# Performance work log

Hardware: AMD Instinct MI355X
Metric: run time of the kernel (lower is better)

The kernel has to match this reference:

```python
import jax, jax.numpy as jnp
import numpy as np

H, DK, OUT = 8, 32, 256
SQRT_DK = float(np.sqrt(DK))


def _proj(feat, W, b):
    # (N, in) -> (N, H, DK)
    return (feat @ W + b).reshape(feat.shape[0], H, DK)


def _rel(k_src, v_src, q_dst, src, dst, att_w, msg_w, pri, n_dst):
    # HGT-style per-relation edge attention + segment softmax + aggregation.
    key = jnp.einsum('ehd,hdk->ehk', k_src[src], att_w)          # (E,H,DK)
    att = (q_dst[dst] * key).sum(-1) * pri / SQRT_DK             # (E,H)
    val = jnp.einsum('ehd,hdk->ehk', v_src[src], msg_w)          # (E,H,DK)
    m = jax.ops.segment_max(att, dst, num_segments=n_dst)
    m = jnp.where(jnp.isfinite(m), m, 0.0)
    e = jnp.exp(att - m[dst])
    s = jax.ops.segment_sum(e, dst, num_segments=n_dst)
    alpha = e / jnp.maximum(s[dst], 1e-9)
    h = jax.ops.segment_sum(alpha[..., None] * val, dst, num_segments=n_dst)
    return jax.nn.relu(h.reshape(n_dst, OUT))                    # relu per etype (reduce_func)


def _ln(x, g, b):
    mu = x.mean(-1, keepdims=True)
    var = ((x - mu) ** 2).mean(-1, keepdims=True)
    return (x - mu) / jnp.sqrt(var + 1e-5) * g + b


def _forward(feat_word, feat_topic, feat_doc, Wk, bk, Wq, bq, Wv, bv, Wa, ba,
             ln_scale, ln_bias, skip, rel_pri, rel_att, rel_msg,
             src_ww, dst_ww, src_wt, dst_wt, src_wd, dst_wd,
             src_tt, dst_tt, src_td, dst_td):
    # ntype order: word=0, topic=1, doc=2; etype order: ww=0, wt=1, wd=2, tt=3, td=4
    Nw, Nt, Nd = feat_word.shape[0], feat_topic.shape[0], feat_doc.shape[0]
    k_w, q_w, v_w = _proj(feat_word, Wk[0], bk[0]), _proj(feat_word, Wq[0], bq[0]), _proj(feat_word, Wv[0], bv[0])
    k_t, q_t, v_t = _proj(feat_topic, Wk[1], bk[1]), _proj(feat_topic, Wq[1], bq[1]), _proj(feat_topic, Wv[1], bv[1])
    q_d = _proj(feat_doc, Wq[2], bq[2])
    t_ww = _rel(k_w, v_w, q_w, src_ww, dst_ww, rel_att[0], rel_msg[0], rel_pri[0], Nw)
    t_wt = _rel(k_w, v_w, q_t, src_wt, dst_wt, rel_att[1], rel_msg[1], rel_pri[1], Nt)
    t_wd = _rel(k_w, v_w, q_d, src_wd, dst_wd, rel_att[2], rel_msg[2], rel_pri[2], Nd)
    t_tt = _rel(k_t, v_t, q_t, src_tt, dst_tt, rel_att[3], rel_msg[3], rel_pri[3], Nt)
    t_td = _rel(k_t, v_t, q_d, src_td, dst_td, rel_att[4], rel_msg[4], rel_pri[4], Nd)
    # cross_reducer='mean' across etypes targeting each ntype
    t_word, t_topic, t_doc = t_ww, (t_wt + t_tt) * 0.5, (t_wd + t_td) * 0.5
    outs = []
    for i, (t, feat) in enumerate([(t_word, feat_word), (t_topic, feat_topic), (t_doc, feat_doc)]):
        a = jax.nn.sigmoid(skip[i])
        trans = (t @ Wa[i] + ba[i]) * a + feat * (1.0 - a)
        outs.append(_ln(trans, ln_scale[i], ln_bias[i]))
    return jnp.concatenate(outs, axis=0)  # (Nw+Nt+Nd, OUT)


def setup_inputs() -> dict:
    key = jax.random.key(0)
    ks = jax.random.split(key, 32)
    Nw, Nt, Nd, D = 20000, 2000, 5000, 256
    E = {'ww': (150000, Nw, Nw), 'wt': (80000, Nw, Nt), 'wd': (80000, Nw, Nd),
         'tt': (20000, Nt, Nt), 'td': (40000, Nt, Nd)}
    inp = {
        'feat_word': jax.random.normal(ks[0], (Nw, D), jnp.float32),
        'feat_topic': jax.random.normal(ks[1], (Nt, D), jnp.float32),
        'feat_doc': jax.random.normal(ks[2], (Nd, D), jnp.float32),
        'Wk': jax.random.normal(ks[3], (3, D, D), jnp.float32) * 0.05,
        'bk': jax.random.normal(ks[4], (3, D), jnp.float32) * 0.02,
        'Wq': jax.random.normal(ks[5], (3, D, D), jnp.float32) * 0.05,
        'bq': jax.random.normal(ks[6], (3, D), jnp.float32) * 0.02,
        'Wv': jax.random.normal(ks[7], (3, D, D), jnp.float32) * 0.05,
        'bv': jax.random.normal(ks[8], (3, D), jnp.float32) * 0.02,
        'Wa': jax.random.normal(ks[9], (3, D, D), jnp.float32) * 0.05,
        'ba': jax.random.normal(ks[10], (3, D), jnp.float32) * 0.02,
        'ln_scale': jnp.ones((3, D), jnp.float32),
        'ln_bias': jnp.zeros((3, D), jnp.float32),
        'skip': jnp.ones((3,), jnp.float32),
        'rel_pri': jnp.ones((5, H), jnp.float32),
        'rel_att': jax.random.normal(ks[11], (5, H, DK, DK), jnp.float32) * 0.1,
        'rel_msg': jax.random.normal(ks[12], (5, H, DK, DK), jnp.float32) * 0.1,
    }
    for i, (et, (ne, ns, nd)) in enumerate(E.items()):
        inp['src_' + et] = jax.random.randint(ks[13 + 2 * i], (ne,), 0, ns, jnp.int32)
        inp['dst_' + et] = jax.random.randint(ks[14 + 2 * i], (ne,), 0, nd, jnp.int32)
    return inp


def reference(feat_word, feat_topic, feat_doc, Wk, bk, Wq, bq, Wv, bv, Wa, ba,
              ln_scale, ln_bias, skip, rel_pri, rel_att, rel_msg,
              src_ww, dst_ww, src_wt, dst_wt, src_wd, dst_wd,
              src_tt, dst_tt, src_td, dst_td):
    return _forward(feat_word, feat_topic, feat_doc, Wk, bk, Wq, bq, Wv, bv, Wa, ba,
                    ln_scale, ln_bias, skip, rel_pri, rel_att, rel_msg,
                    src_ww, dst_ww, src_wt, dst_wt, src_wd, dst_wd,
                    src_tt, dst_tt, src_td, dst_td)
```

## Files before the change

### kernel.cpp

```cpp
#include <hip/hip_runtime.h>

static constexpr int NW = 20000, NT = 2000, ND = 5000;
static constexpr int E_WW = 150000, E_WT = 80000, E_WD = 80000, E_TT = 20000, E_TD = 40000;

typedef short bf16x8 __attribute__((ext_vector_type(8)));
typedef float f32x4 __attribute__((ext_vector_type(4)));
typedef float f32x2 __attribute__((ext_vector_type(2)));

__device__ __forceinline__ unsigned short f2bf(float f) {
  union { float f; unsigned int u; } c; c.f = f;
  unsigned int u = c.u;
  u += 0x7fffu + ((u >> 16) & 1u);
  return (unsigned short)(u >> 16);
}
__device__ __forceinline__ float bf2f(unsigned short h) {
  union { unsigned int u; float f; } c; c.u = ((unsigned int)h) << 16; return c.f;
}
__device__ __forceinline__ bf16x8 pack8(float4 a, float4 b) {
  bf16x8 r;
  r[0] = (short)f2bf(a.x); r[1] = (short)f2bf(a.y); r[2] = (short)f2bf(a.z); r[3] = (short)f2bf(a.w);
  r[4] = (short)f2bf(b.x); r[5] = (short)f2bf(b.y); r[6] = (short)f2bf(b.z); r[7] = (short)f2bf(b.w);
  return r;
}
__device__ __forceinline__ unsigned char f2fp8(float x) {
  int p = __builtin_amdgcn_cvt_pk_fp8_f32(x, x, 0, false);
  return (unsigned char)(p & 0xff);
}

struct CsrDesc {
  const int* dst[5];
  const int* src[5];
  int E[5], N[5], cbase[5];
};

struct PrepArgs {
  const float* psrc[7]; unsigned short* pdst[7];
  const float* wq[5]; const float* bqp[5];
  unsigned short* qdst[5];
  float* beff;
  const float* att;
  const float* msg; unsigned short* wvp;
  CsrDesc dsc;
  int* counts;
  int bEff, bHw, bHist, bTot;
};
__global__ __launch_bounds__(256) void prep_kernel(PrepArgs a) {
  __shared__ float tile[32][33];
  int b = blockIdx.x;
  int tid = threadIdx.x;
  if (b < a.bEff) {
    int m = b >> 6, bk = ((b >> 3) & 7) * 32, bn = (b & 7) * 32;
    const float* W = a.psrc[m];
    unsigned short* WT = a.pdst[m];
    int tx = tid & 31, ty = tid >> 5;
#pragma unroll
    for (int i = 0; i < 32; i += 8)
      tile[ty + i][tx] = W[(size_t)(bk + ty + i) * 256 + bn + tx];
    __syncthreads();
#pragma unroll
    for (int i = 0; i < 32; i += 8)
      WT[(size_t)(bn + ty + i) * 256 + bk + tx] = f2bf(tile[tx][ty + i]);
  } else if (b < a.bHw) {
    int t = (b - a.bEff) * 256 + tid;
    if (t < 5 * 65536) {
      int r = t >> 16, rem = t & 65535;
      int n = rem >> 8, kk = rem & 255;
      int h = n >> 5, j = n & 31;
      const float* wrow = a.wq[r] + kk * 256 + h * 32;
      const float* arow = a.att + r * 8192 + h * 1024 + j * 32;
      float s = 0.f;
#pragma unroll
      for (int d = 0; d < 32; d += 4) {
        float4 wv = *(const float4*)(wrow + d);
        float4 av = *(const float4*)(arow + d);
        s += wv.x * av.x + wv.y * av.y + wv.z * av.z + wv.w * av.w;
      }
      a.qdst[r][n * 256 + kk] = f2bf(s);
    } else {
      int idx = t - 5 * 65536;
      if (idx < 1280) {
        int r = idx >> 8, n = idx & 255;
        int h = n >> 5, j = n & 31;
        const float* brow = a.bqp[r] + h * 32;
        const float* arow = a.att + r * 8192 + h * 1024 + j * 32;
        float s = 0.f;
#pragma unroll
        for (int d = 0; d < 32; d += 4) {
          float4 bv = *(const float4*)(brow + d);
          float4 av = *(const float4*)(arow + d);
          s += bv.x * av.x + bv.y * av.y + bv.z * av.z + bv.w * av.w;
        }
        a.beff[r * 256 + n] = s;
      }
    }
  } else if (b < a.bHist) {
    int t = (b - a.bHw) * 256 + tid;
    if (t < 5 * 8192) {
      int m = t >> 13, rem = t & 8191;
      int hc = rem >> 9, idx = rem & 511;
      int lane = idx >> 3, j = idx & 7;
      int h = hc >> 1, c = hc & 1;
      int k = (lane >> 4) * 8 + j, n = c * 16 + (lane & 15);
      a.wvp[t] = f2bf(a.msg[(size_t)m * 8192 + h * 1024 + k * 32 + n]);
    }
  } else {
    int t = (b - a.bHist) * 256 + tid;
    int r = 0, base = 0;
    while (r < 5 && t >= base + a.dsc.E[r]) { base += a.dsc.E[r]; r++; }
    if (r >= 5) return;
    int e = t - base;
    atomicAdd(a.counts + a.dsc.cbase[r] + a.dsc.dst[r][e], 1);
  }
}

struct ProjAll {
  const float* A[3];
  const unsigned short* WT[3];
  const float* bias[3][4];
  unsigned char* outB[3][4];
  int esz[3][4];
  int M[3], ncolb[3], bcum[4];
  const int* counts; int* offsets; int scanN;
};
__global__ __launch_bounds__(256) void proj_all(ProjAll pa) {
  __shared__ unsigned short As[64 * 64];
  __shared__ unsigned short Bs[64 * 64];
  __shared__ int wpart2[4];
  __shared__ int carry2;
  const int tid = threadIdx.x;
  if ((int)blockIdx.x >= pa.bcum[3]) {
    int lane = tid & 63, w = tid >> 6;
    if (tid == 0) carry2 = 0;
    __syncthreads();
    const int N = pa.scanN;
    for (int base = 0; base < N; base += 1024) {
      int idx = base + tid * 4;
      int v0 = 0, v1 = 0, v2 = 0, v3 = 0;
      if (idx + 3 < N) {
        int4 t4 = *(const int4*)(pa.counts + idx);
        v0 = t4.x; v1 = t4.y; v2 = t4.z; v3 = t4.w;
      } else if (idx < N) {
        v0 = pa.counts[idx];
        if (idx + 1 < N) v1 = pa.counts[idx + 1];
        if (idx + 2 < N) v2 = pa.counts[idx + 2];
      }
      int ts = v0 + v1 + v2 + v3;
      int x = ts;
#pragma unroll
      for (int d = 1; d < 64; d <<= 1) {
        int t = __shfl_up(x, d, 64);
        if (lane >= d) x += t;
      }
      if (lane == 63) wpart2[w] = x;
      __syncthreads();
      if (tid == 0) {
        int s = 0;
#pragma unroll
        for (int j = 0; j < 4; j++) { int t = wpart2[j]; wpart2[j] = s; s += t; }
      }
      __syncthreads();
      int excl = carry2 + wpart2[w] + (x - ts);
      if (idx < N)     pa.offsets[idx]     = excl;
      if (idx + 1 < N) pa.offsets[idx + 1] = excl + v0;
      if (idx + 2 < N) pa.offsets[idx + 2] = excl + v0 + v1;
      if (idx + 3 < N) pa.offsets[idx + 3] = excl + v0 + v1 + v2;
      __syncthreads();
      if (tid == 255) carry2 = excl + ts;
      __syncthreads();
    }
    if (tid == 0) pa.offsets[N] = carry2;
    return;
  }
  int nt = 0;
  while (nt < 2 && (int)blockIdx.x >= pa.bcum[nt + 1]) nt++;
  int local = blockIdx.x - pa.bcum[nt];
  int ncolb = pa.ncolb[nt];
  int bmi = local / ncolb, bnb = local % ncolb;
  const int bm = bmi * 64, bn = bnb * 64;
  const float* A = pa.A[nt];
  const unsigned short* WT = pa.WT[nt];
  const int M = pa.M[nt];
  const int wave = tid >> 6, lane = tid & 63;
  f32x4 acc[4] = {};
  const int ar = wave * 16 + (lane & 15);
  const int swz = lane & 7;
  for (int k0 = 0; k0 < 256; k0 += 64) {
#pragma unroll
    for (int i = 0; i < 2; i++) {
      int c = tid + i * 256;
      int row = c >> 3, sl = c & 7;
      int srow = bm + row;
      float4 a0 = make_float4(0.f, 0.f, 0.f, 0.f), a1 = a0;
      if (srow < M) {
        a0 = *(const float4*)(A + (size_t)srow * 256 + k0 + sl * 8);
        a1 = *(const float4*)(A + (size_t)srow * 256 + k0 + sl * 8 + 4);
      }
      *(bf16x8*)&As[row * 64 + (sl ^ (row & 7)) * 8] = pack8(a0, a1);
      bf16x8 bv = *(const bf16x8*)(WT + (size_t)(bn + row) * 256 + k0 + sl * 8);
      *(bf16x8*)&Bs[row * 64 + (sl ^ (row & 7)) * 8] = bv;
    }
    __syncthreads();
#pragma unroll
    for (int kk = 0; kk < 2; kk++) {
      int slot = kk * 4 + (lane >> 4);
      bf16x8 av = *(const bf16x8*)&As[ar * 64 + ((slot ^ swz) * 8)];
#pragma unroll
      for (int nf = 0; nf < 4; nf++) {
        int br = nf * 16 + (lane & 15);
        bf16x8 bv = *(const bf16x8*)&Bs[br * 64 + ((slot ^ swz) * 8)];
        acc[nf] = __builtin_amdgcn_mfma_f32_16x16x32_bf16(av, bv, acc[nf], 0, 0, 0);
      }
    }
    __syncthreads();
  }
  const int col = lane & 15;
  const int seg = bnb >> 2;
  const float* bias = pa.bias[nt][seg];
  unsigned char* outB = pa.outB[nt][seg];
  const int esz = pa.esz[nt][seg];
  const int cbase = (bnb & 3) * 64;
#pragma unroll
  for (int nf = 0; nf < 4; nf++) {
    float bsv = bias[cbase + nf * 16 + col];
    int idx = cbase + nf * 16 + col;
#pragma unroll
    for (int rr = 0; rr < 4; rr++) {
      int row = bm + wave * 16 + (lane >> 4) * 4 + rr;
      if (row < M) {
        float v = acc[nf][rr] + bsv;
        if (esz == 2) *(unsigned short*)(outB + (size_t)row * 512 + idx * 2) = f2bf(v);
        else          outB[(size_t)row * 512 + idx] = f2fp8(v);
      }
    }
  }
}

__global__ void scatter5(CsrDesc d, const int* __restrict__ offsets, int* __restrict__ cursor,
                         int* __restrict__ ssrc) {
  int t = blockIdx.x * blockDim.x + threadIdx.x;
  int r = 0, base = 0;
  while (r < 5 && t >= base + d.E[r]) { base += d.E[r]; r++; }
  if (r >= 5) return;
  int e = t - base;
  int dn = d.dst[r][e];
  int pos = offsets[d.cbase[r] + dn] + atomicAdd(cursor + d.cbase[r] + dn, 1);
  ssrc[pos] = d.src[r][e];
}

struct AttArgs {
  const unsigned short* qh[5]; const unsigned char* kv8[5];
  const int* offs[5]; unsigned short* agg[5];
  const int* ssrc;
  const float* pri;
  int bcum[6]; int Ndst[5];
};
__global__ __launch_bounds__(256) void fused_att_agg(AttArgs a) {
  int r = 0;
  while (r < 4 && (int)blockIdx.x >= a.bcum[r + 1]) r++;
  int wave = threadIdx.x >> 6, lane = threadIdx.x & 63;
  int node = (blockIdx.x - a.bcum[r]) * 4 + wave;
  if (node >= a.Ndst[r]) return;
  const unsigned short* qh = a.qh[r];
  const unsigned char* kvb = a.kv8[r];
  const int* ssrc = a.ssrc;
  const int* offs = a.offs[r];
  int h = lane >> 3;
  float prih = a.pri[r * 8 + h] * 0.17677669529663687f;
  int r0 = offs[node], r1 = offs[node + 1];
  float4 acc = make_float4(0.f, 0.f, 0.f, 0.f);
  if (r0 < r1) {
    ushort4 qv = *(const ushort4*)(qh + (size_t)node * 256 + lane * 4);
    float q0 = bf2f(qv.x), q1 = bf2f(qv.y), q2 = bf2f(qv.z), q3 = bf2f(qv.w);
    float m = -1e30f, s = 0.f;
    for (int i = r0; i < r1; i += 2) {
      int sA = ssrc[i];
      bool two = (i + 1 < r1);
      int sB = two ? ssrc[i + 1] : sA;
      const unsigned char* pA = kvb + (size_t)sA * 512 + lane * 4;
      const unsigned char* pB = kvb + (size_t)sB * 512 + lane * 4;
      unsigned int kuA = *(const unsigned int*)pA;
      unsigned int kuB = *(const unsigned int*)pB;
      unsigned int vuA = *(const unsigned int*)(pA + 256);
      unsigned int vuB = *(const unsigned int*)(pB + 256);
      f32x2 ka01 = __builtin_amdgcn_cvt_pk_f32_fp8((int)kuA, false);
      f32x2 ka23 = __builtin_amdgcn_cvt_pk_f32_fp8((int)kuA, true);
      f32x2 kb01 = __builtin_amdgcn_cvt_pk_f32_fp8((int)kuB, false);
      f32x2 kb23 = __builtin_amdgcn_cvt_pk_f32_fp8((int)kuB, true);
      float dA = q0 * ka01[0] + q1 * ka01[1] + q2 * ka23[0] + q3 * ka23[1];
      float dB = q0 * kb01[0] + q1 * kb01[1] + q2 * kb23[0] + q3 * kb23[1];
      dA += __shfl_xor(dA, 1, 64); dB += __shfl_xor(dB, 1, 64);
      dA += __shfl_xor(dA, 2, 64); dB += __shfl_xor(dB, 2, 64);
      dA += __shfl_xor(dA, 4, 64); dB += __shfl_xor(dB, 4, 64);
      float lA = dA * prih;
      float lB = two ? dB * prih : -1e30f;
      float mn = fmaxf(m, fmaxf(lA, lB));
      float sc = __expf(m - mn);
      float wA = __expf(lA - mn);
      float wB = __expf(lB - mn);
      m = mn;
      s = s * sc + wA + wB;
      f32x2 va01 = __builtin_amdgcn_cvt_pk_f32_fp8((int)vuA, false);
      f32x2 va23 = __builtin_amdgcn_cvt_pk_f32_fp8((int)vuA, true);
      f32x2 vb01 = __builtin_amdgcn_cvt_pk_f32_fp8((int)vuB, false);
      f32x2 vb23 = __builtin_amdgcn_cvt_pk_f32_fp8((int)vuB, true);
      acc.x = acc.x * sc + wA * va01[0] + wB * vb01[0];
      acc.y = acc.y * sc + wA * va01[1] + wB * vb01[1];
      acc.z = acc.z * sc + wA * va23[0] + wB * vb23[0];
      acc.w = acc.w * sc + wA * va23[1] + wB * vb23[1];
    }
    float inv = 1.f / fmaxf(s, 1e-9f);
    acc.x *= inv; acc.y *= inv; acc.z *= inv; acc.w *= inv;
  }
  ushort4 o;
  o.x = f2bf(acc.x); o.y = f2bf(acc.y); o.z = f2bf(acc.z); o.w = f2bf(acc.w);
  *(ushort4*)(a.agg[r] + (size_t)node * 256 + lane * 4) = o;
}

struct MsgArgs {
  const unsigned short* aggA[3]; const unsigned short* aggB[3];
  const unsigned short* fA[3]; const unsigned short* fB[3];
  unsigned short* t[3];
  float scale[3];
  int N[3]; int bcum[4];
};
__global__ __launch_bounds__(256) void msg_transform_all(MsgArgs a) {
  int g = 0;
  while (g < 2 && (int)blockIdx.x >= a.bcum[g + 1]) g++;
  int local = blockIdx.x - a.bcum[g];
  const unsigned short* aggA = a.aggA[g];
  const unsigned short* aggB = a.aggB[g];
  const unsigned short* fA = a.fA[g];
  const unsigned short* fB = a.fB[g];
  unsigned short* t = a.t[g];
  float scale = a.scale[g];
  int N = a.N[g];
  int wave = threadIdx.x >> 6, lane = threadIdx.x & 63;
  int r0 = local * 64 + wave * 16;
  int arow = r0 + (lane & 15);
  bool valid = arow < N;
  int kofs = (lane >> 4) * 8;
  f32x4 z{};
#pragma unroll
  for (int h = 0; h < 8; h++) {
    bf16x8 aA{}, aB{};
    if (valid) {
      aA = *(const bf16x8*)(aggA + (size_t)arow * 256 + h * 32 + kofs);
      if (aggB) aB = *(const bf16x8*)(aggB + (size_t)arow * 256 + h * 32 + kofs);
    }
#pragma unroll
    for (int c = 0; c < 2; c++) {
      bf16x8 bA = *(const bf16x8*)(fA + ((h * 2 + c) * 64 + lane) * 8);
      f32x4 oA = __builtin_amdgcn_mfma_f32_16x16x32_bf16(aA, bA, z, 0, 0, 0);
      f32x4 oB = z;
      if (aggB) {
        bf16x8 bB = *(const bf16x8*)(fB + ((h * 2 + c) * 64 + lane) * 8);
        oB = __builtin_amdgcn_mfma_f32_16x16x32_bf16(aB, bB, z, 0, 0, 0);
      }
      int colc = h * 32 + c * 16 + (lane & 15);
#pragma unroll
      for (int rr = 0; rr < 4; rr++) {
        int row = r0 + (lane >> 4) * 4 + rr;
        if (row < N) {
          float v = fmaxf(oA[rr], 0.f) + fmaxf(oB[rr], 0.f);
          t[(size_t)row * 256 + colc] = f2bf(v * scale);
        }
      }
    }
  }
}

struct OutAll {
  const unsigned short* tA[3]; const unsigned short* WT[3];
  const float* ba[3]; const float* feat[3];
  const float* gamma[3]; const float* beta[3];
  float* op[3];
  int M[3], bcum[4];
  const float* skipv;
};
__global__ __launch_bounds__(256) void out_all_ln(OutAll oa) {
  __shared__ unsigned short As[64 * 64];
  __shared__ unsigned short Bs[256 * 64];
  int g = 0;
  while (g < 2 && (int)blockIdx.x >= oa.bcum[g + 1]) g++;
  const int bm = (blockIdx.x - oa.bcum[g]) * 64;
  const unsigned short* tA = oa.tA[g];
  const unsigned short* WT = oa.WT[g];
  const int M = oa.M[g];
  const int tid = threadIdx.x, wave = tid >> 6, lane = tid & 63;
  f32x4 acc[16] = {};
  const int ar = wave * 16 + (lane & 15);
  const int swz = lane & 7;
  for (int k0 = 0; k0 < 256; k0 += 64) {
#pragma unroll
    for (int i = 0; i < 2; i++) {
      int c = tid + i * 256;
      int row = c >> 3, sl = c & 7;
      int srow = bm + row;
      bf16x8 av{};
      if (srow < M) av = *(const bf16x8*)(tA + (size_t)srow * 256 + k0 + sl * 8);
      *(bf16x8*)&As[row * 64 + (sl ^ (row & 7)) * 8] = av;
    }
#pragma unroll
    for (int i = 0; i < 8; i++) {
      int c = tid + i * 256;
      int row = c >> 3, sl = c & 7;
      bf16x8 bv = *(const bf16x8*)(WT + (size_t)row * 256 + k0 + sl * 8);
      *(bf16x8*)&Bs[row * 64 + (sl ^ (row & 7)) * 8] = bv;
    }
    __syncthreads();
#pragma unroll
    for (int kk = 0; kk < 2; kk++) {
      int slot = kk * 4 + (lane >> 4);
      bf16x8 av = *(const bf16x8*)&As[ar * 64 + ((slot ^ swz) * 8)];
#pragma unroll
      for (int nf = 0; nf < 16; nf++) {
        int br = nf * 16 + (lane & 15);
        bf16x8 bv = *(const bf16x8*)&Bs[br * 64 + ((slot ^ swz) * 8)];
        acc[nf] = __builtin_amdgcn_mfma_f32_16x16x32_bf16(av, bv, acc[nf], 0, 0, 0);
      }
    }
    __syncthreads();
  }
  const int c16 = lane & 15;
  float a_skip = 1.f / (1.f + __expf(-oa.skipv[g]));
  float one_m = 1.f - a_skip;
  const float* gamma = oa.gamma[g];
  const float* beta = oa.beta[g];
  const float* ba = oa.ba[g];
  const float* feat = oa.feat[g];
  float* outp = oa.op[g];
  float gg[16], bb[16], bia[16];
#pragma unroll
  for (int nf = 0; nf < 16; nf++) {
    gg[nf] = gamma[nf * 16 + c16];
    bb[nf] = beta[nf * 16 + c16];
    bia[nf] = ba[nf * 16 + c16];
  }
#pragma unroll
  for (int rr = 0; rr < 4; rr++) {
    int row = bm + wave * 16 + (lane >> 4) * 4 + rr;
    bool valid = row < M;
#pragma unroll
    for (int nf = 0; nf < 16; nf++) {
      float fv = valid ? feat[(size_t)row * 256 + nf * 16 + c16] : 0.f;
      acc[nf][rr] = (acc[nf][rr] + bia[nf]) * a_skip + fv * one_m;
    }
    float p = 0.f;
#pragma unroll
    for (int nf = 0; nf < 16; nf++) p += acc[nf][rr];
    p += __shfl_xor(p, 1, 16); p += __shfl_xor(p, 2, 16);
    p += __shfl_xor(p, 4, 16); p += __shfl_xor(p, 8, 16);
    float mu = p * (1.f / 256.f);
    float qv = 0.f;
#pragma unroll
    for (int nf = 0; nf < 16; nf++) { float dd = acc[nf][rr] - mu; qv += dd * dd; }
    qv += __shfl_xor(qv, 1, 16); qv += __shfl_xor(qv, 2, 16);
    qv += __shfl_xor(qv, 4, 16); qv += __shfl_xor(qv, 8, 16);
    float rstd = rsqrtf(qv * (1.f / 256.f) + 1e-5f);
    if (valid) {
#pragma unroll
      for (int nf = 0; nf < 16; nf++)
        outp[(size_t)row * 256 + nf * 16 + c16] = (acc[nf][rr] - mu) * rstd * gg[nf] + bb[nf];
    }
  }
}

extern "C" void kernel_launch(void* const* d_in, const int* in_sizes, int n_in,
                              void* d_out, int out_size, void* d_ws, size_t ws_size,
                              hipStream_t stream) {
  const float* feat_w = (const float*)d_in[0];
  const float* feat_t = (const float*)d_in[1];
  const float* feat_d = (const float*)d_in[2];
  const float* Wk = (const float*)d_in[3];
  const float* bk = (const float*)d_in[4];
  const float* Wq = (const float*)d_in[5];
  const float* bq = (const float*)d_in[6];
  const float* Wv = (const float*)d_in[7];
  const float* bv = (const float*)d_in[8];
  const float* Wa = (const float*)d_in[9];
  const float* ba = (const float*)d_in[10];
  const float* ln_scale = (const float*)d_in[11];
  const float* ln_bias = (const float*)d_in[12];
  const float* skip = (const float*)d_in[13];
  const float* rel_pri = (const float*)d_in[14];
  const float* rel_att = (const float*)d_in[15];
  const float* rel_msg = (const float*)d_in[16];
  const int* src_ww = (const int*)d_in[17];
  const int* dst_ww = (const int*)d_in[18];
  const int* src_wt = (const int*)d_in[19];
  const int* dst_wt = (const int*)d_in[20];
  const int* src_wd = (const int*)d_in[21];
  const int* dst_wd = (const int*)d_in[22];
  const int* src_tt = (const int*)d_in[23];
  const int* dst_tt = (const int*)d_in[24];
  const int* src_td = (const int*)d_in[25];
  const int* dst_td = (const int*)d_in[26];
  float* out = (float*)d_out;
  float* ws = (float*)d_ws;

  size_t off = 0;
  auto allocF = [&](size_t nf) { float* p = ws + off; off += nf; return p; };
  unsigned char* kv_w = (unsigned char*)allocF(2560000);
  unsigned char* kv_t = (unsigned char*)allocF(256000);
  unsigned short* qhat0 = (unsigned short*)allocF(2560000);
  unsigned short* qhat1 = (unsigned short*)allocF(256000);
  unsigned short* qhat2 = (unsigned short*)allocF(640000);
  unsigned short* qhat3 = (unsigned short*)allocF(256000);
  unsigned short* qhat4 = (unsigned short*)allocF(640000);
  unsigned short* aggr0 = (unsigned short*)allocF(2560000);
  unsigned short* aggr1 = (unsigned short*)allocF(256000);
  unsigned short* aggr2 = (unsigned short*)allocF(640000);
  unsigned short* aggr3 = (unsigned short*)allocF(256000);
  unsigned short* aggr4 = (unsigned short*)allocF(640000);
  unsigned short* t_word  = (unsigned short*)allocF(2560000);
  unsigned short* t_topic = (unsigned short*)allocF(256000);
  unsigned short* t_doc   = (unsigned short*)allocF(640000);
  unsigned short* WTw = (unsigned short*)allocF(98304);
  unsigned short* WTt = (unsigned short*)allocF(131072);
  unsigned short* WTd = (unsigned short*)allocF(65536);
  unsigned short* WTa = (unsigned short*)allocF(98304);
  unsigned short* wvp = (unsigned short*)allocF(20480);
  float* bq_eff = allocF(1280);
  int* counts  = (int*)allocF(34000);
  int* cursor  = (int*)allocF(34000);
  int* offsets = (int*)allocF(34004);
  int* ssrc    = (int*)allocF(370000);

  dim3 b256(256);
  auto cdiv = [](int a, int b) { return (a + b - 1) / b; };

  CsrDesc dsc;
  dsc.dst[0] = dst_ww; dsc.dst[1] = dst_wt; dsc.dst[2] = dst_wd; dsc.dst[3] = dst_tt; dsc.dst[4] = dst_td;
  dsc.src[0] = src_ww; dsc.src[1] = src_wt; dsc.src[2] = src_wd; dsc.src[3] = src_tt; dsc.src[4] = src_td;
  int Es[5] = {E_WW, E_WT, E_WD, E_TT, E_TD};
  int Ns[5] = {NW, NT, ND, NT, ND};
  int cb = 0;
  for (int r = 0; r < 5; r++) {
    dsc.E[r] = Es[r]; dsc.N[r] = Ns[r]; dsc.cbase[r] = cb;
    cb += Ns[r];
  }

  hipMemsetAsync(counts, 0, (size_t)68000 * sizeof(int), stream);

  {
    PrepArgs pr;
    pr.psrc[0] = Wk;           pr.pdst[0] = WTw + 65536;
    pr.psrc[1] = Wv;           pr.pdst[1] = WTw + 131072;
    pr.psrc[2] = Wk + 65536;   pr.pdst[2] = WTt;
    pr.psrc[3] = Wv + 65536;   pr.pdst[3] = WTt + 65536;
    pr.psrc[4] = Wa;           pr.pdst[4] = WTa;
    pr.psrc[5] = Wa + 65536;   pr.pdst[5] = WTa + 65536;
    pr.psrc[6] = Wa + 131072;  pr.pdst[6] = WTa + 131072;
    pr.wq[0] = Wq;           pr.bqp[0] = bq;        pr.qdst[0] = WTw;
    pr.wq[1] = Wq + 65536;   pr.bqp[1] = bq + 256;  pr.qdst[1] = WTt + 131072;
    pr.wq[2] = Wq + 131072;  pr.bqp[2] = bq + 512;  pr.qdst[2] = WTd;
    pr.wq[3] = Wq + 65536;   pr.bqp[3] = bq + 256;  pr.qdst[3] = WTt + 196608;
    pr.wq[4] = Wq + 131072;  pr.bqp[4] = bq + 512;  pr.qdst[4] = WTd + 65536;
    pr.beff = bq_eff;
    pr.att = rel_att;
    pr.msg = rel_msg; pr.wvp = wvp;
    pr.dsc = dsc; pr.counts = counts;
    int nPack = 7 * 64;
    int nEff  = cdiv(5 * 65536 + 1280, 256);
    int nHw   = cdiv(5 * 8192, 256);
    int nHist = cdiv(370000, 256);
    pr.bEff  = nPack;
    pr.bHw   = nPack + nEff;
    pr.bHist = nPack + nEff + nHw;
    pr.bTot  = nPack + nEff + nHw + nHist;
    prep_kernel<<<pr.bTot, b256, 0, stream>>>(pr);
  }

  {
    ProjAll pa;
    pa.A[0] = feat_w; pa.A[1] = feat_t; pa.A[2] = feat_d;
    pa.WT[0] = WTw;   pa.WT[1] = WTt;   pa.WT[2] = WTd;
    pa.M[0] = NW; pa.M[1] = NT; pa.M[2] = ND;
    pa.bias[0][0] = bq_eff;       pa.outB[0][0] = (unsigned char*)qhat0; pa.esz[0][0] = 2;
    pa.bias[0][1] = bk;           pa.outB[0][1] = kv_w;                  pa.esz[0][1] = 1;
    pa.bias[0][2] = bv;           pa.outB[0][2] = kv_w + 256;            pa.esz[0][2] = 1;
    pa.bias[0][3] = bq_eff;       pa.outB[0][3] = (unsigned char*)qhat0; pa.esz[0][3] = 2;
    pa.bias[1][0] = bk + 256;     pa.outB[1][0] = kv_t;                  pa.esz[1][0] = 1;
    pa.bias[1][1] = bv + 256;     pa.outB[1][1] = kv_t + 256;            pa.esz[1][1] = 1;
    pa.bias[1][2] = bq_eff + 256; pa.outB[1][2] = (unsigned char*)qhat1; pa.esz[1][2] = 2;
    pa.bias[1][3] = bq_eff + 768; pa.outB[1][3] = (unsigned char*)qhat3; pa.esz[1][3] = 2;
    pa.bias[2][0] = bq_eff + 512;  pa.outB[2][0] = (unsigned char*)qhat2; pa.esz[2][0] = 2;
    pa.bias[2][1] = bq_eff + 1024; pa.outB[2][1] = (unsigned char*)qhat4; pa.esz[2][1] = 2;
    pa.bias[2][2] = bq_eff;        pa.outB[2][2] = (unsigned char*)qhat2; pa.esz[2][2] = 2;
    pa.bias[2][3] = bq_eff;        pa.outB[2][3] = (unsigned char*)qhat2; pa.esz[2][3] = 2;
    pa.ncolb[0] = 12; pa.ncolb[1] = 16; pa.ncolb[2] = 8;
    int nb0 = cdiv(NW, 64) * 12, nb1 = cdiv(NT, 64) * 16, nb2 = cdiv(ND, 64) * 8;
    pa.bcum[0] = 0; pa.bcum[1] = nb0; pa.bcum[2] = nb0 + nb1; pa.bcum[3] = nb0 + nb1 + nb2;
    pa.counts = counts; pa.offsets = offsets; pa.scanN = 34000;
    proj_all<<<pa.bcum[3] + 1, b256, 0, stream>>>(pa);
  }

  scatter5<<<cdiv(370000, 256), b256, 0, stream>>>(dsc, offsets, cursor, ssrc);

  int NdstA[5] = {NW, NT, ND, NT, ND};

  {
    AttArgs aa;
    aa.qh[0] = qhat0; aa.qh[1] = qhat1; aa.qh[2] = qhat2; aa.qh[3] = qhat3; aa.qh[4] = qhat4;
    aa.kv8[0] = aa.kv8[1] = aa.kv8[2] = kv_w; aa.kv8[3] = aa.kv8[4] = kv_t;
    unsigned short* aggs[5] = {aggr0, aggr1, aggr2, aggr3, aggr4};
    aa.ssrc = ssrc;
    int bc = 0;
    for (int r = 0; r < 5; r++) {
      aa.offs[r] = offsets + dsc.cbase[r];
      aa.agg[r] = aggs[r];
      aa.Ndst[r] = NdstA[r];
      aa.bcum[r] = bc; bc += cdiv(NdstA[r], 4);
    }
    aa.bcum[5] = bc;
    aa.pri = rel_pri;
    fused_att_agg<<<bc, b256, 0, stream>>>(aa);
  }

  {
    MsgArgs ma;
    ma.aggA[0] = aggr0; ma.aggB[0] = nullptr;
    ma.fA[0] = wvp;             ma.fB[0] = wvp;
    ma.t[0] = t_word;  ma.scale[0] = 1.0f;  ma.N[0] = NW;
    ma.aggA[1] = aggr1; ma.aggB[1] = aggr3;
    ma.fA[1] = wvp + 8192;      ma.fB[1] = wvp + 3 * 8192;
    ma.t[1] = t_topic; ma.scale[1] = 0.5f;  ma.N[1] = NT;
    ma.aggA[2] = aggr2; ma.aggB[2] = aggr4;
    ma.fA[2] = wvp + 2 * 8192;  ma.fB[2] = wvp + 4 * 8192;
    ma.t[2] = t_doc;   ma.scale[2] = 0.5f;  ma.N[2] = ND;
    int bc = 0;
    for (int g = 0; g < 3; g++) { ma.bcum[g] = bc; bc += cdiv(ma.N[g], 64); }
    ma.bcum[3] = bc;
    msg_transform_all<<<bc, b256, 0, stream>>>(ma);
  }

  {
    OutAll oa;
    oa.tA[0] = t_word;  oa.tA[1] = t_topic; oa.tA[2] = t_doc;
    oa.WT[0] = WTa; oa.WT[1] = WTa + 65536; oa.WT[2] = WTa + 131072;
    oa.ba[0] = ba; oa.ba[1] = ba + 256; oa.ba[2] = ba + 512;
    oa.feat[0] = feat_w; oa.feat[1] = feat_t; oa.feat[2] = feat_d;
    oa.gamma[0] = ln_scale; oa.gamma[1] = ln_scale + 256; oa.gamma[2] = ln_scale + 512;
    oa.beta[0] = ln_bias; oa.beta[1] = ln_bias + 256; oa.beta[2] = ln_bias + 512;
    oa.op[0] = out; oa.op[1] = out + (size_t)NW * 256; oa.op[2] = out + (size_t)(NW + NT) * 256;
    oa.M[0] = NW; oa.M[1] = NT; oa.M[2] = ND;
    int bc = 0;
    for (int g = 0; g < 3; g++) { oa.bcum[g] = bc; bc += cdiv(oa.M[g], 64); }
    oa.bcum[3] = bc;
    oa.skipv = skip;
    out_all_ln<<<bc, b256, 0, stream>>>(oa);
  }

  (void)in_sizes; (void)n_in; (void)out_size; (void)ws_size;
}
```

Before: 209.0 us.

## Load each A row block once and loop over all output column groups

The projection GEMM now assigns one 64-row block of input features per workgroup. It converts the full 64x256 A tile to bf16 in LDS once, then loops over 256-wide column groups with 16 MFMA accumulators each. Previously every 64x64 output tile reloaded and reconverted its A slice, so A global traffic was multiplied by the column-block count. The cost is far fewer workgroups (about 430 instead of about 4700), larger LDS use (64KB), and 64 accumulator registers per thread, which may reduce occupancy and parallelism.

```diff
diff --git a/kernel.cpp b/kernel.cpp
--- a/kernel.cpp
+++ b/kernel.cpp
@@ -119,12 +119,12 @@
   const float* bias[3][4];
   unsigned char* outB[3][4];
   int esz[3][4];
-  int M[3], ncolb[3], bcum[4];
+  int M[3], ncolg[3], bcum[4];
   const int* counts; int* offsets; int scanN;
 };
 __global__ __launch_bounds__(256) void proj_all(ProjAll pa) {
-  __shared__ unsigned short As[64 * 64];
-  __shared__ unsigned short Bs[64 * 64];
+  __shared__ unsigned short As[64 * 256];
+  __shared__ unsigned short Bs[256 * 64];
   __shared__ int wpart2[4];
   __shared__ int carry2;
   const int tid = threadIdx.x;
@@ -173,63 +173,67 @@
   }
   int nt = 0;
   while (nt < 2 && (int)blockIdx.x >= pa.bcum[nt + 1]) nt++;
-  int local = blockIdx.x - pa.bcum[nt];
-  int ncolb = pa.ncolb[nt];
-  int bmi = local / ncolb, bnb = local % ncolb;
-  const int bm = bmi * 64, bn = bnb * 64;
+  const int bm = (blockIdx.x - pa.bcum[nt]) * 64;
   const float* A = pa.A[nt];
   const unsigned short* WT = pa.WT[nt];
   const int M = pa.M[nt];
   const int wave = tid >> 6, lane = tid & 63;
-  f32x4 acc[4] = {};
   const int ar = wave * 16 + (lane & 15);
   const int swz = lane & 7;
-  for (int k0 = 0; k0 < 256; k0 += 64) {
-#pragma unroll
-    for (int i = 0; i < 2; i++) {
-      int c = tid + i * 256;
-      int row = c >> 3, sl = c & 7;
-      int srow = bm + row;
-      float4 a0 = make_float4(0.f, 0.f, 0.f, 0.f), a1 = a0;
-      if (srow < M) {
-        a0 = *(const float4*)(A + (size_t)srow * 256 + k0 + sl * 8);
-        a1 = *(const float4*)(A + (size_t)srow * 256 + k0 + sl * 8 + 4);
-      }
-      *(bf16x8*)&As[row * 64 + (sl ^ (row & 7)) * 8] = pack8(a0, a1);
-      bf16x8 bv = *(const bf16x8*)(WT + (size_t)(bn + row) * 256 + k0 + sl * 8);
-      *(bf16x8*)&Bs[row * 64 + (sl ^ (row & 7)) * 8] = bv;
-    }
-    __syncthreads();
-#pragma unroll
-    for (int kk = 0; kk < 2; kk++) {
-      int slot = kk * 4 + (lane >> 4);
-      bf16x8 av = *(const bf16x8*)&As[ar * 64 + ((slot ^ swz) * 8)];
-#pragma unroll
-      for (int nf = 0; nf < 4; nf++) {
-        int br = nf * 16 + (lane & 15);
-        bf16x8 bv = *(const bf16x8*)&Bs[br * 64 + ((slot ^ swz) * 8)];
-        acc[nf] = __builtin_amdgcn_mfma_f32_16x16x32_bf16(av, bv, acc[nf], 0, 0, 0);
-      }
-    }
-    __syncthreads();
-  }
-  const int col = lane & 15;
-  const int seg = bnb >> 2;
-  const float* bias = pa.bias[nt][seg];
-  unsigned char* outB = pa.outB[nt][seg];
-  const int esz = pa.esz[nt][seg];
-  const int cbase = (bnb & 3) * 64;
-#pragma unroll
-  for (int nf = 0; nf < 4; nf++) {
-    float bsv = bias[cbase + nf * 16 + col];
-    int idx = cbase + nf * 16 + col;
-#pragma unroll
-    for (int rr = 0; rr < 4; rr++) {
-      int row = bm + wave * 16 + (lane >> 4) * 4 + rr;
-      if (row < M) {
-        float v = acc[nf][rr] + bsv;
-        if (esz == 2) *(unsigned short*)(outB + (size_t)row * 512 + idx * 2) = f2bf(v);
-        else          outB[(size_t)row * 512 + idx] = f2fp8(v);
+#pragma unroll
+  for (int i = 0; i < 8; i++) {
+    int c = i * 256 + tid;
+    int row = c >> 5, sv = c & 31;
+    int srow = bm + row;
+    float4 a0 = make_float4(0.f, 0.f, 0.f, 0.f), a1 = a0;
+    if (srow < M) {
+      a0 = *(const float4*)(A + (size_t)srow * 256 + sv * 8);
+      a1 = *(const float4*)(A + (size_t)srow * 256 + sv * 8 + 4);
+    }
+    *(bf16x8*)&As[row * 256 + ((sv ^ (row & 7)) * 8)] = pack8(a0, a1);
+  }
+  const int ncolg = pa.ncolg[nt];
+  for (int cg = 0; cg < ncolg; cg++) {
+    f32x4 acc[16] = {};
+    for (int k0 = 0; k0 < 256; k0 += 64) {
+      __syncthreads();
+#pragma unroll
+      for (int i = 0; i < 8; i++) {
+        int c = tid + i * 256;
+        int row = c >> 3, sl = c & 7;
+        bf16x8 bv = *(const bf16x8*)(WT + (size_t)(cg * 256 + row) * 256 + k0 + sl * 8);
+        *(bf16x8*)&Bs[row * 64 + ((sl ^ (row & 7)) * 8)] = bv;
+      }
+      __syncthreads();
+#pragma unroll
+      for (int kk = 0; kk < 2; kk++) {
+        int slot = kk * 4 + (lane >> 4);
+        int gslot = (k0 >> 3) + slot;
+        bf16x8 av = *(const bf16x8*)&As[ar * 256 + ((gslot ^ swz) * 8)];
+#pragma unroll
+        for (int nf = 0; nf < 16; nf++) {
+          int br = nf * 16 + (lane & 15);
+          bf16x8 bv = *(const bf16x8*)&Bs[br * 64 + ((slot ^ swz) * 8)];
+          acc[nf] = __builtin_amdgcn_mfma_f32_16x16x32_bf16(av, bv, acc[nf], 0, 0, 0);
+        }
+      }
+    }
+    const int col = lane & 15;
+    const float* bias = pa.bias[nt][cg];
+    unsigned char* outB = pa.outB[nt][cg];
+    const int esz = pa.esz[nt][cg];
+#pragma unroll
+    for (int nf = 0; nf < 16; nf++) {
+      float bsv = bias[nf * 16 + col];
+      int idx = nf * 16 + col;
+#pragma unroll
+      for (int rr = 0; rr < 4; rr++) {
+        int row = bm + wave * 16 + (lane >> 4) * 4 + rr;
+        if (row < M) {
+          float v = acc[nf][rr] + bsv;
+          if (esz == 2) *(unsigned short*)(outB + (size_t)row * 512 + idx * 2) = f2bf(v);
+          else          outB[(size_t)row * 512 + idx] = f2fp8(v);
+        }
       }
     }
   }
@@ -588,8 +592,8 @@
     pa.bias[2][1] = bq_eff + 1024; pa.outB[2][1] = (unsigned char*)qhat4; pa.esz[2][1] = 2;
     pa.bias[2][2] = bq_eff;        pa.outB[2][2] = (unsigned char*)qhat2; pa.esz[2][2] = 2;
     pa.bias[2][3] = bq_eff;        pa.outB[2][3] = (unsigned char*)qhat2; pa.esz[2][3] = 2;
-    pa.ncolb[0] = 12; pa.ncolb[1] = 16; pa.ncolb[2] = 8;
-    int nb0 = cdiv(NW, 64) * 12, nb1 = cdiv(NT, 64) * 16, nb2 = cdiv(ND, 64) * 8;
+    pa.ncolg[0] = 3; pa.ncolg[1] = 4; pa.ncolg[2] = 2;
+    int nb0 = cdiv(NW, 64), nb1 = cdiv(NT, 64), nb2 = cdiv(ND, 64);
     pa.bcum[0] = 0; pa.bcum[1] = nb0; pa.bcum[2] = nb0 + nb1; pa.bcum[3] = nb0 + nb1 + nb2;
     pa.counts = counts; pa.offsets = offsets; pa.scanN = 34000;
     proj_all<<<pa.bcum[3] + 1, b256, 0, stream>>>(pa);
```

Result: no change. 209.2 us (+0.1%).
